# Kernel optimization log

Measured on AMD Instinct MI355X. Metric: run time of the kernel, lower is better.

Reference implementation:

```python
import jax, jax.numpy as jnp
import numpy as np

T_SEG = 8      # n_segment
KSZ = 3        # LAM temporal kernel size
PAD = 1        # LAM temporal padding
BN_EPS = 1e-5


def setup_inputs() -> dict:
    key = jax.random.key(0)
    ks = jax.random.split(key, 12)
    n, t, c, h, w = 8, T_SEG, 256, 56, 56
    return {
        "x": jax.random.normal(ks[0], (n * t, c, h, w), jnp.float32),
        "net_w": jax.random.normal(ks[1], (c, c, 3, 3), jnp.float32) * 0.02,
        "net_b": jax.random.normal(ks[2], (c,), jnp.float32) * 0.02,
        "lam_w": jax.random.normal(ks[3], (c, c), jnp.float32) * 0.02,
        "lam_b": jax.random.normal(ks[4], (c,), jnp.float32) * 0.02,
        "mlp_w1": jax.random.normal(ks[5], (2 * t, t), jnp.float32) * 0.3,
        "bn_gamma": jax.random.uniform(ks[6], (2 * t,), jnp.float32, 0.5, 1.5),
        "bn_beta": jax.random.normal(ks[7], (2 * t,), jnp.float32) * 0.1,
        "bn_mean": jax.random.normal(ks[8], (2 * t,), jnp.float32) * 0.1,
        "bn_var": jax.random.uniform(ks[9], (2 * t,), jnp.float32, 0.5, 1.5),
        "mlp_w2": jax.random.normal(ks[10], (KSZ, 2 * t), jnp.float32) * 0.3,
        "me_w": jax.random.normal(ks[11], (3,), jnp.float32) * 0.3,
    }


def reference(x, net_w, net_b, lam_w, lam_b, mlp_w1, bn_gamma, bn_beta,
              bn_mean, bn_var, mlp_w2, me_w):
    t = T_SEG
    nt, c, h, w = x.shape
    n = nt // t

    # --- wrapped net: Conv2d 3x3, pad 1 ---
    out = jax.lax.conv_general_dilated(
        x, net_w, window_strides=(1, 1), padding="SAME",
        dimension_numbers=("NCHW", "OIHW", "NCHW"))
    out = out + net_b[None, :, None, None]

    # --- LAM ---
    new_x = out.reshape(n, t, c, h, w).transpose(0, 2, 1, 3, 4)  # (n,c,t,h,w)
    x_g = new_x.mean(axis=(2, 3, 4))                   # global pool -> (n,c)
    x_g = x_g @ lam_w.T + lam_b                        # Conv1d k=1 == matmul
    new_x = new_x + x_g[:, :, None, None, None]

    pooled = new_x.mean(axis=(3, 4)).reshape(n * c, t)  # per-(n,c) temporal sig
    hdn = pooled @ mlp_w1.T                              # (n*c, 2t), no bias
    hdn = (hdn - bn_mean) * (bn_gamma / jnp.sqrt(bn_var + BN_EPS)) + bn_beta
    hdn = jax.nn.relu(hdn)
    wgt = jax.nn.softmax(hdn @ mlp_w2.T, axis=-1).reshape(n, c, KSZ)

    # grouped conv2d (groups=n*c) == per-(n,c) depthwise temporal conv
    xpad = jnp.pad(new_x, ((0, 0), (0, 0), (PAD, PAD), (0, 0), (0, 0)))
    lam_out = sum(wgt[:, :, k, None, None, None] * xpad[:, :, k:k + t]
                  for k in range(KSZ))                  # (n,c,t,h,w)
    lam_out = lam_out.transpose(0, 2, 1, 3, 4).reshape(nt, c, h, w)

    # --- ME ---
    xv = lam_out.reshape(n, t, c, h, w)
    diff = xv[:, 1:] - xv[:, :-1]                       # frame differences
    diff = jnp.pad(diff, ((0, 0), (0, 1), (0, 0), (0, 0), (0, 0)))
    diff = diff.reshape(nt, c, h, w)
    y = diff.mean(axis=(2, 3))                          # (nt, c)
    ypad = jnp.pad(y, ((0, 0), (1, 1)))                 # conv1d over channel dim
    yc = sum(me_w[k] * ypad[:, k:k + c] for k in range(3))
    gate = jax.nn.sigmoid(yc)[:, :, None, None]

    return gate * lam_out
```

## Files before the change

### kernel.cpp

```cpp
#include <hip/hip_runtime.h>
#include <hip/hip_bf16.h>
#include <stdint.h>

#define AS1 __attribute__((address_space(1)))
#define AS3 __attribute__((address_space(3)))

typedef __attribute__((ext_vector_type(8))) short short8v;
typedef __attribute__((ext_vector_type(4))) float float4v;

#define NT 64
#define CCH 256
#define HH 56
#define WW 56
#define HWSZ 3136
#define HP 58
#define WP 58

#define OFF_XT   0ull
#define SZ_XT    110231552ull
#define OFF_WPK  (OFF_XT + SZ_XT)
#define SZ_WPK   1179648ull
#define OFF_CS   (OFF_WPK + SZ_WPK)
#define SZ_CS    65536ull
#define OFF_XG2  (OFF_CS + SZ_CS)
#define SZ_XG2   8192ull
#define OFF_WGT  (OFF_XG2 + SZ_XG2)
#define SZ_WGT   24576ull
#define OFF_M    (OFF_WGT + SZ_WGT)
#define SZ_M     65536ull
#define OFF_GATE (OFF_M + SZ_M)
#define SZ_GATE  65536ull

__device__ __forceinline__ unsigned short f2bf(float f) {
    unsigned int u = __float_as_uint(f);
    unsigned int r = (u + 0x7fffu + ((u >> 16) & 1u)) >> 16;
    return (unsigned short)r;
}

__device__ __forceinline__ void gload16(const unsigned short* g, unsigned short* l) {
    __builtin_amdgcn_global_load_lds((const AS1 void*)g, (AS3 void*)l, 16, 0, 0);
}

__global__ __launch_bounds__(256) void k0_transpose(const float* __restrict__ x,
                                                    unsigned short* __restrict__ xt) {
    int b = blockIdx.x;
    int cb = b & 3;
    int h  = (b >> 2) % 56;
    int nt = b / (4 * 56);
    int c0 = cb * 64;
    int tid = threadIdx.x;

    __shared__ float xs[64 * 57];

    const float* src = x + ((size_t)nt * CCH + c0) * HWSZ + h * WW;
    for (int li = tid; li < 896; li += 256) {
        int row = li / 14, f4 = li % 14;
        float4v v = *(const float4v*)(src + (size_t)row * HWSZ + f4 * 4);
        float* d = &xs[row * 57 + f4 * 4];
        d[0] = v.x; d[1] = v.y; d[2] = v.z; d[3] = v.w;
    }
    __syncthreads();

    unsigned short* dst = xt + (((size_t)nt * HP + (h + 1)) * WP) * CCH + c0;
    for (int job = tid; job < 464; job += 256) {
        int ww = job >> 3, cg = job & 7;
        short8v v;
        if (ww == 0 || ww == 57) {
            v = (short8v){0,0,0,0,0,0,0,0};
        } else {
            #pragma unroll
            for (int jj = 0; jj < 8; ++jj)
                v[jj] = (short)f2bf(xs[(cg * 8 + jj) * 57 + (ww - 1)]);
        }
        *(short8v*)(dst + ww * CCH + cg * 8) = v;
    }
    if (h == 0) {
        unsigned short* d0  = xt + ((size_t)nt * HP + 0)  * WP * CCH + c0;
        unsigned short* d57 = xt + ((size_t)nt * HP + 57) * WP * CCH + c0;
        short8v z = (short8v){0,0,0,0,0,0,0,0};
        for (int job = tid; job < 464; job += 256) {
            int ww = job >> 3, cg = job & 7;
            *(short8v*)(d0  + ww * CCH + cg * 8) = z;
            *(short8v*)(d57 + ww * CCH + cg * 8) = z;
        }
    }
}

__global__ __launch_bounds__(256) void kw_pack(const float* __restrict__ nw,
                                               unsigned short* __restrict__ wpk) {
    int idx = blockIdx.x * 256 + threadIdx.x;
    int rs = idx >> 16;
    int k  = (idx >> 8) & 255;
    int c  = idx & 255;
    wpk[idx] = f2bf(nw[(k * 256 + c) * 9 + rs]);
}


#define STG(nb, h, tA, tB) do { \
    gload16(wpk + (tA) + aoffs[h][0], &lds[(nb) * 16384 + ldst[h][0]]); \
    gload16(xt  + (tB) + boffs[h][0], &lds[32768 + (nb) * 16384 + ldst[h][0]]); \
    gload16(wpk + (tA) + aoffs[h][1], &lds[(nb) * 16384 + ldst[h][1]]); \
    gload16(xt  + (tB) + boffs[h][1], &lds[32768 + (nb) * 16384 + ldst[h][1]]); \
} while (0)

#define LDA8(row, kk) (*(const short8v*)&lds[abase + (row) * 64 + ((((kk) * 4 + hi) ^ xk) << 3)])
#define LDB8(row, kk) (*(const short8v*)&lds[bbase + (row) * 64 + ((((kk) * 4 + hi) ^ xk) << 3)])

#define QUAD2(qq) do { \
    const int _r0 = wm * 128 + (qq) * 64 + r16; \
    short8v _a0k0 = LDA8(_r0, 0),      _a0k1 = LDA8(_r0, 1); \
    short8v _a1k0 = LDA8(_r0 + 16, 0), _a1k1 = LDA8(_r0 + 16, 1); \
    short8v _a2k0 = LDA8(_r0 + 32, 0), _a2k1 = LDA8(_r0 + 32, 1); \
    short8v _a3k0 = LDA8(_r0 + 48, 0), _a3k1 = LDA8(_r0 + 48, 1); \
    asm volatile("s_waitcnt lgkmcnt(0)" ::: "memory"); \
    __builtin_amdgcn_sched_barrier(0); \
    __builtin_amdgcn_s_setprio(1); \
    _Pragma("unroll") \
    for (int _j = 0; _j < 4; ++_j) { \
        acc[(qq) * 4 + 0][_j] = __builtin_amdgcn_mfma_f32_16x16x32_bf16(_a0k0, bfrag[_j][0], acc[(qq) * 4 + 0][_j], 0, 0, 0); \
        acc[(qq) * 4 + 1][_j] = __builtin_amdgcn_mfma_f32_16x16x32_bf16(_a1k0, bfrag[_j][0], acc[(qq) * 4 + 1][_j], 0, 0, 0); \
        acc[(qq) * 4 + 2][_j] = __builtin_amdgcn_mfma_f32_16x16x32_bf16(_a2k0, bfrag[_j][0], acc[(qq) * 4 + 2][_j], 0, 0, 0); \
        acc[(qq) * 4 + 3][_j] = __builtin_amdgcn_mfma_f32_16x16x32_bf16(_a3k0, bfrag[_j][0], acc[(qq) * 4 + 3][_j], 0, 0, 0); \
        acc[(qq) * 4 + 0][_j] = __builtin_amdgcn_mfma_f32_16x16x32_bf16(_a0k1, bfrag[_j][1], acc[(qq) * 4 + 0][_j], 0, 0, 0); \
        acc[(qq) * 4 + 1][_j] = __builtin_amdgcn_mfma_f32_16x16x32_bf16(_a1k1, bfrag[_j][1], acc[(qq) * 4 + 1][_j], 0, 0, 0); \
        acc[(qq) * 4 + 2][_j] = __builtin_amdgcn_mfma_f32_16x16x32_bf16(_a2k1, bfrag[_j][1], acc[(qq) * 4 + 2][_j], 0, 0, 0); \
        acc[(qq) * 4 + 3][_j] = __builtin_amdgcn_mfma_f32_16x16x32_bf16(_a3k1, bfrag[_j][1], acc[(qq) * 4 + 3][_j], 0, 0, 0); \
    } \
    __builtin_amdgcn_s_setprio(0); \
} while (0)

#define BARSYNC do { \
    __builtin_amdgcn_s_barrier(); \
    __builtin_amdgcn_sched_barrier(0); \
} while (0)

__global__ __launch_bounds__(512, 2) void conv_mfma(const unsigned short* __restrict__ xt,
                                                    const unsigned short* __restrict__ wpk,
                                                    const float* __restrict__ net_b,
                                                    float* __restrict__ out,
                                                    float* __restrict__ chansum) {
    __shared__ unsigned short lds[65536];

    const int tid  = threadIdx.x;
    const int lane = tid & 63;
    const int wid  = tid >> 6;
    const int wm   = wid >> 2;
    const int wp   = wid & 3;
    const int r16  = lane & 15;
    const int hi   = lane >> 4;
    const int xk   = r16 & 7;

    const int pblk = (blockIdx.x & 7) * 98 + (blockIdx.x >> 3);
    const int p0 = pblk * 256;

    int aoffs[2][2]; long boffs[2][2]; int ldst[2][2];
    #pragma unroll
    for (int h = 0; h < 2; ++h) {
        #pragma unroll
        for (int ld = 0; ld < 2; ++ld) {
            int ch = wid * 128 + ld * 64 + lane;
            int rr = ch >> 3;
            int kc = (ch & 7) ^ (rr & 7);
            aoffs[h][ld] = (h * 128 + rr) * 256 + kc * 8;
            int p = p0 + h * 128 + rr;
            int nt = p / HWSZ, hw = p - nt * HWSZ;
            int hh = hw / WW,  w  = hw - hh * WW;
            boffs[h][ld] = ((long)(nt * HP + hh) * WP + w) * 256 + kc * 8;
            ldst[h][ld] = h * 8192 + (wid * 128 + ld * 64) * 8;
        }
    }

    float4v acc[8][4];
    #pragma unroll
    for (int i = 0; i < 8; ++i)
        #pragma unroll
        for (int j = 0; j < 4; ++j) acc[i][j] = (float4v){0.f, 0.f, 0.f, 0.f};

    STG(0, 0, 0, 0);
    STG(0, 1, 0, 0);

    for (int kt = 0; kt < 36; ++kt) {
        const int abase = (kt & 1) * 16384;
        const int bbase = 32768 + abase;
        const int nb = (kt & 1) ^ 1;
        const int ktn = kt + 1;
        const bool pf = ktn < 36;
        int tAn = 0, tBn = 0;
        if (pf) {
            const int rsn = ktn >> 2, con = (ktn & 3) * 64;
            tAn = rsn * 65536 + con;
            tBn = ((rsn / 3) * WP + (rsn - (rsn / 3) * 3)) * 256 + con;
        }

        if (pf) {
            STG(nb, 0, tAn, tBn);
            asm volatile("s_waitcnt vmcnt(4)" ::: "memory");
        } else {
            asm volatile("s_waitcnt vmcnt(0)" ::: "memory");
        }
        BARSYNC;

        short8v bfrag[4][2];
        #pragma unroll
        for (int j = 0; j < 4; ++j) {
            const int br = wp * 64 + j * 16 + r16;
            bfrag[j][0] = LDB8(br, 0);
            bfrag[j][1] = LDB8(br, 1);
        }
        QUAD2(0);
        if (pf) STG(nb, 1, tAn, tBn);
        QUAD2(1);
        BARSYNC;
    }

    const int pw = p0 + wp * 64;
    const int ntw = pw / HWSZ;
    const int hwb = pw - ntw * HWSZ;
    #pragma unroll
    for (int mi = 0; mi < 8; ++mi) {
        #pragma unroll
        for (int r = 0; r < 4; ++r) {
            const int m = wm * 128 + mi * 16 + hi * 4 + r;
            const float bias = net_b[m];
            float csum = 0.f;
            float* orow = out + ((size_t)ntw * CCH + m) * HWSZ + hwb;
            #pragma unroll
            for (int j = 0; j < 4; ++j) {
                float v = acc[mi][j][r] + bias;
                orow[j * 16 + r16] = v;
                csum += v;
            }
            csum += __shfl_xor(csum, 1);
            csum += __shfl_xor(csum, 2);
            csum += __shfl_xor(csum, 4);
            csum += __shfl_xor(csum, 8);
            if (r16 == 0) atomicAdd(&chansum[ntw * CCH + m], csum);
        }
    }
}

__global__ __launch_bounds__(256) void k2_xg(const float* __restrict__ chansum,
                                             const float* __restrict__ lam_w,
                                             const float* __restrict__ lam_b,
                                             float* __restrict__ xg2) {
    int n = blockIdx.x, c = threadIdx.x;
    __shared__ float xs[256];
    float s = 0.f;
    #pragma unroll
    for (int t = 0; t < 8; ++t) s += chansum[(n * 8 + t) * CCH + c];
    xs[c] = s * (1.0f / (3136.f * 8.f));
    __syncthreads();
    float d = lam_b[c];
    const float* row = lam_w + c * 256;
    for (int cc = 0; cc < 256; ++cc) d += row[cc] * xs[cc];
    xg2[n * 256 + c] = d;
}

__global__ __launch_bounds__(256) void k3_wgt(const float* __restrict__ chansum,
                                              const float* __restrict__ xg2,
                                              const float* __restrict__ w1,
                                              const float* __restrict__ bg,
                                              const float* __restrict__ bb,
                                              const float* __restrict__ bm,
                                              const float* __restrict__ bv,
                                              const float* __restrict__ w2,
                                              float* __restrict__ wgt,
                                              float* __restrict__ mbuf) {
    int idx = blockIdx.x * 256 + threadIdx.x;
    int n = idx >> 8, c = idx & 255;
    float xg = xg2[idx];
    float p[8];
    #pragma unroll
    for (int t = 0; t < 8; ++t)
        p[t] = chansum[(n * 8 + t) * CCH + c] * (1.0f / 3136.f) + xg;
    float hd[16];
    #pragma unroll
    for (int j = 0; j < 16; ++j) {
        float s = 0.f;
        #pragma unroll
        for (int t = 0; t < 8; ++t) s += p[t] * w1[j * 8 + t];
        s = (s - bm[j]) * (bg[j] * rsqrtf(bv[j] + 1e-5f)) + bb[j];
        hd[j] = fmaxf(s, 0.f);
    }
    float lg[3];
    #pragma unroll
    for (int k = 0; k < 3; ++k) {
        float s = 0.f;
        #pragma unroll
        for (int j = 0; j < 16; ++j) s += hd[j] * w2[k * 16 + j];
        lg[k] = s;
    }
    float mx = fmaxf(fmaxf(lg[0], lg[1]), lg[2]);
    float e0 = expf(lg[0] - mx), e1 = expf(lg[1] - mx), e2 = expf(lg[2] - mx);
    float inv = 1.f / (e0 + e1 + e2);
    float wk[3] = {e0 * inv, e1 * inv, e2 * inv};
    #pragma unroll
    for (int k = 0; k < 3; ++k) wgt[idx * 3 + k] = wk[k];
    #pragma unroll
    for (int t = 0; t < 8; ++t) {
        float s = 0.f;
        #pragma unroll
        for (int k = 0; k < 3; ++k) {
            int tt = t + k - 1;
            if (tt >= 0 && tt < 8) s += wk[k] * p[tt];
        }
        mbuf[idx * 8 + t] = s;
    }
}

__global__ __launch_bounds__(256) void k4_gate(const float* __restrict__ mbuf,
                                               const float* __restrict__ me_w,
                                               float* __restrict__ gate) {
    int b = blockIdx.x;
    int n = b >> 3, t = b & 7;
    int c = threadIdx.x;
    __shared__ float y[256];
    float yv = 0.f;
    if (t < 7) yv = mbuf[(n * 256 + c) * 8 + t + 1] - mbuf[(n * 256 + c) * 8 + t];
    y[c] = yv;
    __syncthreads();
    float yc = me_w[1] * yv;
    if (c > 0)   yc += me_w[0] * y[c - 1];
    if (c < 255) yc += me_w[2] * y[c + 1];
    gate[b * 256 + c] = 1.f / (1.f + expf(-yc));
}

__global__ __launch_bounds__(256) void k5_final(float* __restrict__ out,
                                                const float* __restrict__ wgt,
                                                const float* __restrict__ xg2,
                                                const float* __restrict__ gate) {
    int tid = blockIdx.x * 256 + threadIdx.x;
    int hw4 = tid % 784;
    int nc = tid / 784;
    int n = nc >> 8, c = nc & 255;
    float w0 = wgt[nc * 3 + 0], w1 = wgt[nc * 3 + 1], w2 = wgt[nc * 3 + 2];
    float xg = xg2[nc];
    const size_t tstride = (size_t)CCH * HWSZ;
    size_t base = ((size_t)(n * 8) * CCH + c) * HWSZ + hw4 * 4;

    float4v o[8];
    #pragma unroll
    for (int t = 0; t < 8; ++t) o[t] = *(const float4v*)(out + base + t * tstride);

    #pragma unroll
    for (int t = 0; t < 8; ++t) {
        float g = gate[(n * 8 + t) * CCH + c];
        float4v lam;
        #pragma unroll
        for (int q = 0; q < 4; ++q) {
            float v = w1 * (o[t][q] + xg);
            if (t > 0) v += w0 * (o[t - 1][q] + xg);
            if (t < 7) v += w2 * (o[t + 1][q] + xg);
            lam[q] = g * v;
        }
        *(float4v*)(out + base + t * tstride) = lam;
    }
}

extern "C" void kernel_launch(void* const* d_in, const int* in_sizes, int n_in,
                              void* d_out, int out_size, void* d_ws, size_t ws_size,
                              hipStream_t stream) {
    const float* x      = (const float*)d_in[0];
    const float* net_w  = (const float*)d_in[1];
    const float* net_b  = (const float*)d_in[2];
    const float* lam_w  = (const float*)d_in[3];
    const float* lam_b  = (const float*)d_in[4];
    const float* mlp_w1 = (const float*)d_in[5];
    const float* bn_g   = (const float*)d_in[6];
    const float* bn_b   = (const float*)d_in[7];
    const float* bn_m   = (const float*)d_in[8];
    const float* bn_v   = (const float*)d_in[9];
    const float* mlp_w2 = (const float*)d_in[10];
    const float* me_w   = (const float*)d_in[11];
    float* out = (float*)d_out;

    char* ws = (char*)d_ws;
    unsigned short* xt  = (unsigned short*)(ws + OFF_XT);
    unsigned short* wpk = (unsigned short*)(ws + OFF_WPK);
    float* chansum = (float*)(ws + OFF_CS);
    float* xg2     = (float*)(ws + OFF_XG2);
    float* wgt     = (float*)(ws + OFF_WGT);
    float* mbuf    = (float*)(ws + OFF_M);
    float* gate    = (float*)(ws + OFF_GATE);

    hipMemsetAsync(chansum, 0, SZ_CS, stream);
    kw_pack<<<2304, 256, 0, stream>>>(net_w, wpk);
    k0_transpose<<<64 * 56 * 4, 256, 0, stream>>>(x, xt);
    conv_mfma<<<784, 512, 0, stream>>>(xt, wpk, net_b, out, chansum);
    k2_xg<<<8, 256, 0, stream>>>(chansum, lam_w, lam_b, xg2);
    k3_wgt<<<8, 256, 0, stream>>>(chansum, xg2, mlp_w1, bn_g, bn_b, bn_m, bn_v, mlp_w2, wgt, mbuf);
    k4_gate<<<64, 256, 0, stream>>>(mbuf, me_w, gate);
    k5_final<<<6272, 256, 0, stream>>>(out, wgt, xg2, gate);
}
```

Baseline: 461.2 us.

## Split conv MFMA loop into four barrier phases interleaving A/B tile prefetch

The main GEMM loop is now four phases of two 16-row A fragments each, with a barrier before and after each phase. The next tile's global-to-LDS loads are split into four pieces: B half 0 at loop start, then B half 1, A half 0 and A half 1 in phases 1-3. The load mapping is simplified to use thread id directly, and the vmcnt wait drops to 2. The aim is to spread memory traffic more evenly across MFMA work, at the cost of many more workgroup barriers per iteration.

```diff
diff --git a/kernel.cpp b/kernel.cpp
--- a/kernel.cpp
+++ b/kernel.cpp
@@ -96,42 +96,46 @@
 }
 
 
-#define STG(nb, h, tA, tB) do { \
-    gload16(wpk + (tA) + aoffs[h][0], &lds[(nb) * 16384 + ldst[h][0]]); \
-    gload16(xt  + (tB) + boffs[h][0], &lds[32768 + (nb) * 16384 + ldst[h][0]]); \
-    gload16(wpk + (tA) + aoffs[h][1], &lds[(nb) * 16384 + ldst[h][1]]); \
-    gload16(xt  + (tB) + boffs[h][1], &lds[32768 + (nb) * 16384 + ldst[h][1]]); \
+#define STG_A(nb, h, tA) do { \
+    gload16(wpk + (tA) + aoff[h][0], &lds[(nb) * 16384 + (h) * 8192 + ldsd0]); \
+    gload16(wpk + (tA) + aoff[h][1], &lds[(nb) * 16384 + (h) * 8192 + ldsd1]); \
+} while (0)
+
+#define STG_B(nb, h, tB) do { \
+    gload16(xt + (tB) + boff[h][0], &lds[32768 + (nb) * 16384 + (h) * 8192 + ldsd0]); \
+    gload16(xt + (tB) + boff[h][1], &lds[32768 + (nb) * 16384 + (h) * 8192 + ldsd1]); \
 } while (0)
 
 #define LDA8(row, kk) (*(const short8v*)&lds[abase + (row) * 64 + ((((kk) * 4 + hi) ^ xk) << 3)])
 #define LDB8(row, kk) (*(const short8v*)&lds[bbase + (row) * 64 + ((((kk) * 4 + hi) ^ xk) << 3)])
 
-#define QUAD2(qq) do { \
-    const int _r0 = wm * 128 + (qq) * 64 + r16; \
-    short8v _a0k0 = LDA8(_r0, 0),      _a0k1 = LDA8(_r0, 1); \
-    short8v _a1k0 = LDA8(_r0 + 16, 0), _a1k1 = LDA8(_r0 + 16, 1); \
-    short8v _a2k0 = LDA8(_r0 + 32, 0), _a2k1 = LDA8(_r0 + 32, 1); \
-    short8v _a3k0 = LDA8(_r0 + 48, 0), _a3k1 = LDA8(_r0 + 48, 1); \
+#define BARSYNC do { \
+    __builtin_amdgcn_s_barrier(); \
+    __builtin_amdgcn_sched_barrier(0); \
+} while (0)
+
+#define PHASE(p, STAGE_STMT) do { \
+    short8v _a0 = LDA8(wm * 128 + (2 * (p)) * 16 + r16, 0); \
+    short8v _a1 = LDA8(wm * 128 + (2 * (p) + 1) * 16 + r16, 0); \
+    short8v _a2 = LDA8(wm * 128 + (2 * (p)) * 16 + r16, 1); \
+    short8v _a3 = LDA8(wm * 128 + (2 * (p) + 1) * 16 + r16, 1); \
+    STAGE_STMT; \
+    BARSYNC; \
     asm volatile("s_waitcnt lgkmcnt(0)" ::: "memory"); \
     __builtin_amdgcn_sched_barrier(0); \
     __builtin_amdgcn_s_setprio(1); \
     _Pragma("unroll") \
     for (int _j = 0; _j < 4; ++_j) { \
-        acc[(qq) * 4 + 0][_j] = __builtin_amdgcn_mfma_f32_16x16x32_bf16(_a0k0, bfrag[_j][0], acc[(qq) * 4 + 0][_j], 0, 0, 0); \
-        acc[(qq) * 4 + 1][_j] = __builtin_amdgcn_mfma_f32_16x16x32_bf16(_a1k0, bfrag[_j][0], acc[(qq) * 4 + 1][_j], 0, 0, 0); \
-        acc[(qq) * 4 + 2][_j] = __builtin_amdgcn_mfma_f32_16x16x32_bf16(_a2k0, bfrag[_j][0], acc[(qq) * 4 + 2][_j], 0, 0, 0); \
-        acc[(qq) * 4 + 3][_j] = __builtin_amdgcn_mfma_f32_16x16x32_bf16(_a3k0, bfrag[_j][0], acc[(qq) * 4 + 3][_j], 0, 0, 0); \
-        acc[(qq) * 4 + 0][_j] = __builtin_amdgcn_mfma_f32_16x16x32_bf16(_a0k1, bfrag[_j][1], acc[(qq) * 4 + 0][_j], 0, 0, 0); \
-        acc[(qq) * 4 + 1][_j] = __builtin_amdgcn_mfma_f32_16x16x32_bf16(_a1k1, bfrag[_j][1], acc[(qq) * 4 + 1][_j], 0, 0, 0); \
-        acc[(qq) * 4 + 2][_j] = __builtin_amdgcn_mfma_f32_16x16x32_bf16(_a2k1, bfrag[_j][1], acc[(qq) * 4 + 2][_j], 0, 0, 0); \
-        acc[(qq) * 4 + 3][_j] = __builtin_amdgcn_mfma_f32_16x16x32_bf16(_a3k1, bfrag[_j][1], acc[(qq) * 4 + 3][_j], 0, 0, 0); \
+        acc[2 * (p)][_j]     = __builtin_amdgcn_mfma_f32_16x16x32_bf16(_a0, bfrag[_j][0], acc[2 * (p)][_j], 0, 0, 0); \
+        acc[2 * (p) + 1][_j] = __builtin_amdgcn_mfma_f32_16x16x32_bf16(_a1, bfrag[_j][0], acc[2 * (p) + 1][_j], 0, 0, 0); \
+    } \
+    _Pragma("unroll") \
+    for (int _j = 0; _j < 4; ++_j) { \
+        acc[2 * (p)][_j]     = __builtin_amdgcn_mfma_f32_16x16x32_bf16(_a2, bfrag[_j][1], acc[2 * (p)][_j], 0, 0, 0); \
+        acc[2 * (p) + 1][_j] = __builtin_amdgcn_mfma_f32_16x16x32_bf16(_a3, bfrag[_j][1], acc[2 * (p) + 1][_j], 0, 0, 0); \
     } \
     __builtin_amdgcn_s_setprio(0); \
-} while (0)
-
-#define BARSYNC do { \
-    __builtin_amdgcn_s_barrier(); \
-    __builtin_amdgcn_sched_barrier(0); \
+    BARSYNC; \
 } while (0)
 
 __global__ __launch_bounds__(512, 2) void conv_mfma(const unsigned short* __restrict__ xt,
@@ -153,20 +157,22 @@
     const int pblk = (blockIdx.x & 7) * 98 + (blockIdx.x >> 3);
     const int p0 = pblk * 256;
 
-    int aoffs[2][2]; long boffs[2][2]; int ldst[2][2];
-    #pragma unroll
-    for (int h = 0; h < 2; ++h) {
-        #pragma unroll
-        for (int ld = 0; ld < 2; ++ld) {
-            int ch = wid * 128 + ld * 64 + lane;
-            int rr = ch >> 3;
-            int kc = (ch & 7) ^ (rr & 7);
-            aoffs[h][ld] = (h * 128 + rr) * 256 + kc * 8;
-            int p = p0 + h * 128 + rr;
-            int nt = p / HWSZ, hw = p - nt * HWSZ;
-            int hh = hw / WW,  w  = hw - hh * WW;
-            boffs[h][ld] = ((long)(nt * HP + hh) * WP + w) * 256 + kc * 8;
-            ldst[h][ld] = h * 8192 + (wid * 128 + ld * 64) * 8;
+    int aoff[2][2]; long boff[2][2]; int ldsd0, ldsd1;
+    {
+        int chs[2] = { tid, 512 + tid };
+        ldsd0 = chs[0] * 8; ldsd1 = chs[1] * 8;
+        #pragma unroll
+        for (int i = 0; i < 2; ++i) {
+            int rr = chs[i] >> 3;
+            int kc = (chs[i] & 7) ^ (rr & 7);
+            #pragma unroll
+            for (int h = 0; h < 2; ++h) {
+                aoff[h][i] = (h * 128 + rr) * 256 + kc * 8;
+                int p = p0 + h * 128 + rr;
+                int nt = p / HWSZ, hw = p - nt * HWSZ;
+                int hh = hw / WW,  w  = hw - hh * WW;
+                boff[h][i] = ((long)(nt * HP + hh) * WP + w) * 256 + kc * 8;
+            }
         }
     }
 
@@ -176,8 +182,10 @@
         #pragma unroll
         for (int j = 0; j < 4; ++j) acc[i][j] = (float4v){0.f, 0.f, 0.f, 0.f};
 
-    STG(0, 0, 0, 0);
-    STG(0, 1, 0, 0);
+    STG_B(0, 0, 0);
+    STG_B(0, 1, 0);
+    STG_A(0, 0, 0);
+    STG_A(0, 1, 0);
 
     for (int kt = 0; kt < 36; ++kt) {
         const int abase = (kt & 1) * 16384;
@@ -193,8 +201,8 @@
         }
 
         if (pf) {
-            STG(nb, 0, tAn, tBn);
-            asm volatile("s_waitcnt vmcnt(4)" ::: "memory");
+            STG_B(nb, 0, tBn);
+            asm volatile("s_waitcnt vmcnt(2)" ::: "memory");
         } else {
             asm volatile("s_waitcnt vmcnt(0)" ::: "memory");
         }
@@ -207,10 +215,31 @@
             bfrag[j][0] = LDB8(br, 0);
             bfrag[j][1] = LDB8(br, 1);
         }
-        QUAD2(0);
-        if (pf) STG(nb, 1, tAn, tBn);
-        QUAD2(1);
+        {
+            short8v _a0 = LDA8(wm * 128 + 0 * 16 + r16, 0);
+            short8v _a1 = LDA8(wm * 128 + 1 * 16 + r16, 0);
+            short8v _a2 = LDA8(wm * 128 + 0 * 16 + r16, 1);
+            short8v _a3 = LDA8(wm * 128 + 1 * 16 + r16, 1);
+            asm volatile("s_waitcnt lgkmcnt(0)" ::: "memory");
+            __builtin_amdgcn_sched_barrier(0);
+            __builtin_amdgcn_s_setprio(1);
+            #pragma unroll
+            for (int _j = 0; _j < 4; ++_j) {
+                acc[0][_j] = __builtin_amdgcn_mfma_f32_16x16x32_bf16(_a0, bfrag[_j][0], acc[0][_j], 0, 0, 0);
+                acc[1][_j] = __builtin_amdgcn_mfma_f32_16x16x32_bf16(_a1, bfrag[_j][0], acc[1][_j], 0, 0, 0);
+            }
+            #pragma unroll
+            for (int _j = 0; _j < 4; ++_j) {
+                acc[0][_j] = __builtin_amdgcn_mfma_f32_16x16x32_bf16(_a2, bfrag[_j][1], acc[0][_j], 0, 0, 0);
+                acc[1][_j] = __builtin_amdgcn_mfma_f32_16x16x32_bf16(_a3, bfrag[_j][1], acc[1][_j], 0, 0, 0);
+            }
+            __builtin_amdgcn_s_setprio(0);
+        }
         BARSYNC;
+
+        PHASE(1, if (pf) STG_B(nb, 1, tBn));
+        PHASE(2, if (pf) STG_A(nb, 0, tAn));
+        PHASE(3, if (pf) STG_A(nb, 1, tAn));
     }
 
     const int pw = p0 + wp * 64;
```

Measured after the change: 464.2 us. About the same (+0.7%).
